# Kernel tuning notes

Hardware: AMD Instinct MI355X
Metric: run time of the kernel (lower is better)

Reference implementation:

```python
import jax, jax.numpy as jnp
import numpy as np

K_MASK = -2.3819763e+38
B, T, D = 1, 2048, 3584
N, KH, H = 28, 4, 128  # query heads, kv heads, head_dim
ROPE_THETA = 1000000.0


def _rope_tables(t, h, theta):
    pos = jnp.arange(t, dtype=jnp.float32)[:, None]
    freq = theta ** (-jnp.arange(0, h, 2, dtype=jnp.float32) / h)[None, :]
    ang = pos * freq  # (T, H/2)
    return jnp.sin(ang)[None], jnp.cos(ang)[None]  # (1, T, H/2)


def apply_rotary_embedding(x, sin, cos):
    # x: (B,T,heads,H); sin/cos: (B,T,H/2)
    x1, x2 = x[..., : x.shape[-1] // 2], x[..., x.shape[-1] // 2 :]
    s, c = sin[:, :, None, :], cos[:, :, None, :]
    return jnp.concatenate([x1 * c - x2 * s, x2 * c + x1 * s], axis=-1)


def setup_inputs() -> dict:
    key = jax.random.key(0)
    ks = jax.random.split(key, 8)
    x = jax.random.normal(ks[0], (B, T, D), jnp.float32)
    attn_mask = jnp.tril(jnp.ones((T, T), jnp.bool_))[None]  # causal (B,T,S)
    sin, cos = _rope_tables(T, H, ROPE_THETA)
    std = 0.02
    wq = jax.random.normal(ks[1], (D, N, H), jnp.float32) * std
    wk = jax.random.normal(ks[2], (D, KH, H), jnp.float32) * std
    wv = jax.random.normal(ks[3], (D, KH, H), jnp.float32) * std
    wo = jax.random.normal(ks[4], (N, H, D), jnp.float32) * std
    q_bias = jax.random.normal(ks[5], (N * H,), jnp.float32) * std
    k_bias = jax.random.normal(ks[6], (KH * H,), jnp.float32) * std
    v_bias = jax.random.normal(ks[7], (KH * H,), jnp.float32) * std
    return {"x": x, "attn_mask": attn_mask, "sin": sin, "cos": cos,
            "wq": wq, "wk": wk, "wv": wv, "wo": wo,
            "q_bias": q_bias, "k_bias": k_bias, "v_bias": v_bias}


def reference(x, attn_mask, sin, cos, wq, wk, wv, wo, q_bias, k_bias, v_bias):
    b, t, _ = x.shape
    q = jnp.einsum('BTD,DNH->BTNH', x, wq) + q_bias.reshape(1, 1, N, H)
    k = jnp.einsum('BSD,DKH->BSKH', x, wk) + k_bias.reshape(1, 1, KH, H)
    v = jnp.einsum('BSD,DKH->BSKH', x, wv) + v_bias.reshape(1, 1, KH, H)
    q = apply_rotary_embedding(q, sin, cos)
    k = apply_rotary_embedding(k, sin, cos)
    g = N // KH  # GQA group size
    scale = H ** -0.5
    qg = q.reshape(b, t, KH, g, H)
    attn = jnp.einsum('BTHGD,BSHD->BHGTS', qg, k) * scale  # no KV repetition
    attn = attn.reshape(b, N, t, t)
    attn = jnp.where(attn_mask[:, None, :, :], attn, K_MASK)
    attn = jax.nn.softmax(attn.astype(jnp.float32), axis=-1).astype(k.dtype)
    attn = attn.reshape(b, KH, g, t, t)
    qkv = jnp.einsum('BHGTS,BSHD->BTHGD', attn, v).reshape(b, t, N, H)
    return jnp.einsum('BTNH,NHD->BTD', qkv, wo)
```

## Files before the change

### kernel.cpp

```cpp
#include <hip/hip_runtime.h>
#include <hip/hip_bf16.h>
#include <math.h>

#define Tn 2048
#define Dn 3584
#define NH 28
#define KHn 4
#define Hn 128
#define Gn 7
#define SCALE 0.08838834764831845f
#define LDC 4608
#define KOFF 3584
#define VOFF 4096
#define FBQ 128
#define FBS 64

typedef unsigned short u16;
typedef __attribute__((ext_vector_type(8))) short short8;
typedef __attribute__((ext_vector_type(4))) float floatx4;

__device__ __forceinline__ float bf_lo(unsigned int u) {
    union { unsigned int i; float f; } x; x.i = u << 16; return x.f;
}
__device__ __forceinline__ u16 f2bf(float f) {
    __hip_bfloat16 h = __float2bfloat16(f);
    return *reinterpret_cast<u16*>(&h);
}

__global__ void cast_f32_bf16(const float* __restrict__ in, u16* __restrict__ out, int n4)
{
    const int idx = blockIdx.x * blockDim.x + threadIdx.x;
    if (idx >= n4) return;
    const float4 f = ((const float4*)in)[idx];
    ((ushort4*)out)[idx] = make_ushort4(f2bf(f.x), f2bf(f.y), f2bf(f.z), f2bf(f.w));
}

__global__ __launch_bounds__(256) void transpose_cast(
    const float* __restrict__ in, u16* __restrict__ out, int R, int C, int ldo)
{
    __shared__ float ts[32][33];
    const int tid = threadIdx.x;
    const int c0 = blockIdx.x * 32, r0 = blockIdx.y * 32;
    const int tx = tid & 31, ty = tid >> 5;
    #pragma unroll
    for (int i = 0; i < 4; ++i)
        ts[ty + i * 8][tx] = in[(size_t)(r0 + ty + i * 8) * C + c0 + tx];
    __syncthreads();
    #pragma unroll
    for (int i = 0; i < 4; ++i)
        out[(size_t)(c0 + ty + i * 8) * ldo + r0 + tx] = f2bf(ts[tx][ty + i * 8]);
}

__global__ __launch_bounds__(256) void transpose_v(
    const u16* __restrict__ qkv, u16* __restrict__ vt)
{
    __shared__ u16 ts[32][33];
    const int tid = threadIdx.x;
    const int s0 = blockIdx.x * 32, d0 = blockIdx.y * 32;
    const int tx = tid & 31, ty = tid >> 5;
    #pragma unroll
    for (int i = 0; i < 4; ++i)
        ts[ty + i * 8][tx] = qkv[(size_t)(s0 + ty + i * 8) * LDC + VOFF + d0 + tx];
    __syncthreads();
    #pragma unroll
    for (int i = 0; i < 4; ++i)
        vt[(size_t)(d0 + ty + i * 8) * Tn + s0 + tx] = ts[tx][ty + i * 8];
}

__global__ void concat_bias(const float* __restrict__ qb, const float* __restrict__ kb,
                            const float* __restrict__ vb, float* __restrict__ out)
{
    const int j = blockIdx.x * blockDim.x + threadIdx.x;
    if (j >= 4608) return;
    out[j] = j < 3584 ? qb[j] : (j < 4096 ? kb[j - 3584] : vb[j - 4096]);
}

#define GM 128
#define GN 128
#define GK 32

__device__ __forceinline__ void async16(const void* g, void* l) {
    __builtin_amdgcn_global_load_lds(
        (const __attribute__((address_space(1))) unsigned int*)g,
        (__attribute__((address_space(3))) unsigned int*)l, 16, 0, 0);
}

template <typename OUT_T>
__global__ __launch_bounds__(256) void gemm_bf16_mfma(
    const u16* __restrict__ A, const u16* __restrict__ Bt,
    const float* __restrict__ bias, OUT_T* __restrict__ C,
    int M, int N, int K, int ldc)
{
    __shared__ __align__(16) u16 As[GM * GK];
    __shared__ __align__(16) u16 Bs[GN * GK];

    const int tid  = threadIdx.x;
    const int lane = tid & 63;
    const int wave = tid >> 6;
    const int wr = wave >> 1, wc = wave & 1;
    const int m16 = lane & 15, quad = lane >> 4;

    const int bm = blockIdx.y * GM;
    const int bn = blockIdx.x * GN;

    floatx4 acc[4][4];
    #pragma unroll
    for (int i = 0; i < 4; ++i)
        #pragma unroll
        for (int j = 0; j < 4; ++j) acc[i][j] = (floatx4)0.f;

    const int rl   = lane >> 2;
    const int kcol = (lane & 3) * 8;

    for (int k0 = 0; k0 < K; k0 += GK) {
        __syncthreads();
        #pragma unroll
        for (int i = 0; i < 2; ++i) {
            const int c = wave + i * 4;
            const int row = c * 16 + rl;
            async16(A  + (size_t)(bm + row) * K + k0 + kcol, &As[c * 512]);
            async16(Bt + (size_t)(bn + row) * K + k0 + kcol, &Bs[c * 512]);
        }
        __builtin_amdgcn_s_waitcnt(0);
        __syncthreads();

        short8 af[4], bfr[4];
        #pragma unroll
        for (int i = 0; i < 4; ++i)
            af[i] = *(const short8*)&As[(wr * 64 + i * 16 + m16) * GK + quad * 8];
        #pragma unroll
        for (int j = 0; j < 4; ++j)
            bfr[j] = *(const short8*)&Bs[(wc * 64 + j * 16 + m16) * GK + quad * 8];
        #pragma unroll
        for (int i = 0; i < 4; ++i)
            #pragma unroll
            for (int j = 0; j < 4; ++j)
                acc[i][j] = __builtin_amdgcn_mfma_f32_16x16x32_bf16(
                    af[i], bfr[j], acc[i][j], 0, 0, 0);
    }

    #pragma unroll
    for (int j = 0; j < 4; ++j) {
        const int col = bn + wc * 64 + j * 16 + m16;
        const float bv = bias ? bias[col] : 0.f;
        #pragma unroll
        for (int i = 0; i < 4; ++i) {
            const int rbase = bm + wr * 64 + i * 16 + quad * 4;
            #pragma unroll
            for (int r = 0; r < 4; ++r) {
                const float v = acc[i][j][r] + bv;
                if constexpr (sizeof(OUT_T) == 2)
                    C[(size_t)(rbase + r) * ldc + col] = (OUT_T)f2bf(v);
                else
                    C[(size_t)(rbase + r) * ldc + col] = v;
            }
        }
    }
}

__global__ void rope_bf16(u16* __restrict__ base,
                          const float* __restrict__ sin_t,
                          const float* __restrict__ cos_t,
                          int heads)
{
    const int idx = blockIdx.x * blockDim.x + threadIdx.x;
    const int n_elem = Tn * heads * 64;
    if (idx >= n_elem) return;
    const int i = idx & 63;
    const int h = (idx >> 6) % heads;
    const int t = idx / (64 * heads);
    const float s = sin_t[t * 64 + i];
    const float c = cos_t[t * 64 + i];
    u16* p = base + (size_t)t * LDC + h * Hn;
    const float x1 = bf_lo((unsigned int)p[i]);
    const float x2 = bf_lo((unsigned int)p[i + 64]);
    p[i]      = f2bf(x1 * c - x2 * s);
    p[i + 64] = f2bf(x2 * c + x1 * s);
}

__global__ __launch_bounds__(256, 2) void flash_attn_mfma(
    const u16* __restrict__ qkv, const u16* __restrict__ vt, u16* __restrict__ o)
{
    const int qt = (int)(gridDim.x - 1 - blockIdx.x);
    const int n  = blockIdx.y;
    const int kh = n / Gn;
    const int tid  = threadIdx.x;
    const int lane = tid & 63;
    const int w    = tid >> 6;
    const int m16  = lane & 15;
    const int quad = lane >> 4;

    __shared__ __align__(16) u16 smem[64 * 136 + 128 * 72 + 128 * 72];
    u16* Ks = smem;
    u16* Vs = smem + 64 * 136;
    u16* Ps = Vs + 128 * 72;
    u16* Os = smem;

    short8 qf[2][4];
    #pragma unroll
    for (int p = 0; p < 2; ++p) {
        const int qrow = qt * FBQ + w * 32 + p * 16 + m16;
        const u16* qp = qkv + (size_t)qrow * LDC + n * Hn;
        #pragma unroll
        for (int kc = 0; kc < 4; ++kc)
            qf[p][kc] = *(const short8*)(qp + kc * 32 + quad * 8);
    }

    floatx4 oacc[2][8];
    #pragma unroll
    for (int p = 0; p < 2; ++p)
        #pragma unroll
        for (int jn = 0; jn < 8; ++jn) oacc[p][jn] = (floatx4)0.f;
    float mrow[2][4], lrow[2][4];
    #pragma unroll
    for (int p = 0; p < 2; ++p)
        #pragma unroll
        for (int r = 0; r < 4; ++r) { mrow[p][r] = -3.0e38f; lrow[p][r] = 0.f; }

    const int krow = tid >> 2, kseg = tid & 3;
    const int vrow = tid >> 1, vseg = tid & 1;
    const int nst = 2 * qt + 2;

    uint4 kv[4], vv[4];
    {
        const u16* kp = qkv + (size_t)(krow) * LDC + KOFF + kh * Hn + kseg * 32;
        #pragma unroll
        for (int i = 0; i < 4; ++i) kv[i] = *(const uint4*)(kp + i * 8);
        const u16* vp = vt + (size_t)(kh * Hn + vrow) * Tn + vseg * 32;
        #pragma unroll
        for (int i = 0; i < 4; ++i) vv[i] = *(const uint4*)(vp + i * 8);
    }

    for (int st = 0; st < nst; ++st) {
        __syncthreads();
        #pragma unroll
        for (int i = 0; i < 4; ++i)
            *(uint4*)&Ks[krow * 136 + kseg * 32 + i * 8] = kv[i];
        #pragma unroll
        for (int i = 0; i < 4; ++i)
            *(uint4*)&Vs[vrow * 72 + vseg * 32 + i * 8] = vv[i];
        __syncthreads();

        {
            const int pst = (st + 1 < nst) ? st + 1 : nst - 1;
            const u16* kp = qkv + (size_t)(pst * FBS + krow) * LDC + KOFF + kh * Hn + kseg * 32;
            #pragma unroll
            for (int i = 0; i < 4; ++i) kv[i] = *(const uint4*)(kp + i * 8);
            const u16* vp = vt + (size_t)(kh * Hn + vrow) * Tn + pst * FBS + vseg * 32;
            #pragma unroll
            for (int i = 0; i < 4; ++i) vv[i] = *(const uint4*)(vp + i * 8);
        }

        const bool active = (st * FBS) <= (qt * FBQ + w * 32 + 31);
        if (active) {
            floatx4 sacc[2][4];
            #pragma unroll
            for (int p = 0; p < 2; ++p)
                #pragma unroll
                for (int j = 0; j < 4; ++j) sacc[p][j] = (floatx4)0.f;
            #pragma unroll
            for (int j = 0; j < 4; ++j) {
                #pragma unroll
                for (int kc = 0; kc < 4; ++kc) {
                    const short8 bfv = *(const short8*)&Ks[(j * 16 + m16) * 136 + kc * 32 + quad * 8];
                    sacc[0][j] = __builtin_amdgcn_mfma_f32_16x16x32_bf16(qf[0][kc], bfv, sacc[0][j], 0, 0, 0);
                    sacc[1][j] = __builtin_amdgcn_mfma_f32_16x16x32_bf16(qf[1][kc], bfv, sacc[1][j], 0, 0, 0);
                }
            }

            const bool diag = (st >= 2 * qt);
            #pragma unroll
            for (int p = 0; p < 2; ++p) {
                #pragma unroll
                for (int r = 0; r < 4; ++r) {
                    const int prow = w * 32 + p * 16 + quad * 4 + r;
                    const int row  = qt * FBQ + prow;
                    float sv[4];
                    #pragma unroll
                    for (int j = 0; j < 4; ++j) {
                        float s = sacc[p][j][r] * SCALE;
                        if (diag && (st * FBS + j * 16 + m16 > row)) s = -1.0e30f;
                        sv[j] = s;
                    }
                    float mx = fmaxf(fmaxf(sv[0], sv[1]), fmaxf(sv[2], sv[3]));
                    mx = fmaxf(mx, __shfl_xor(mx, 1));
                    mx = fmaxf(mx, __shfl_xor(mx, 2));
                    mx = fmaxf(mx, __shfl_xor(mx, 4));
                    mx = fmaxf(mx, __shfl_xor(mx, 8));
                    const float mnew  = fmaxf(mrow[p][r], mx);
                    const float alpha = __expf(mrow[p][r] - mnew);
                    mrow[p][r] = mnew;
                    float ls = 0.f;
                    #pragma unroll
                    for (int j = 0; j < 4; ++j) {
                        const float e = __expf(sv[j] - mnew);
                        ls += e;
                        Ps[prow * 72 + j * 16 + m16] = f2bf(e);
                    }
                    lrow[p][r] = lrow[p][r] * alpha + ls;
                    #pragma unroll
                    for (int jn = 0; jn < 8; ++jn) oacc[p][jn][r] *= alpha;
                }
            }

            #pragma unroll
            for (int kc2 = 0; kc2 < 2; ++kc2) {
                const short8 af0 = *(const short8*)&Ps[(w * 32 + m16) * 72 + kc2 * 32 + quad * 8];
                const short8 af1 = *(const short8*)&Ps[(w * 32 + 16 + m16) * 72 + kc2 * 32 + quad * 8];
                #pragma unroll
                for (int jn = 0; jn < 8; ++jn) {
                    const short8 bfv = *(const short8*)&Vs[(jn * 16 + m16) * 72 + kc2 * 32 + quad * 8];
                    oacc[0][jn] = __builtin_amdgcn_mfma_f32_16x16x32_bf16(af0, bfv, oacc[0][jn], 0, 0, 0);
                    oacc[1][jn] = __builtin_amdgcn_mfma_f32_16x16x32_bf16(af1, bfv, oacc[1][jn], 0, 0, 0);
                }
            }
        }
    }

    float inv[2][4];
    #pragma unroll
    for (int p = 0; p < 2; ++p)
        #pragma unroll
        for (int r = 0; r < 4; ++r) {
            float l = lrow[p][r];
            l += __shfl_xor(l, 1); l += __shfl_xor(l, 2);
            l += __shfl_xor(l, 4); l += __shfl_xor(l, 8);
            inv[p][r] = 1.0f / l;
        }

    __syncthreads();
    #pragma unroll
    for (int p = 0; p < 2; ++p)
        #pragma unroll
        for (int r = 0; r < 4; ++r) {
            const int mrw = w * 32 + p * 16 + quad * 4 + r;
            #pragma unroll
            for (int jn = 0; jn < 8; ++jn)
                Os[mrw * 136 + jn * 16 + m16] = f2bf(oacc[p][jn][r] * inv[p][r]);
        }
    {
        const int mrw  = w * 32 + (lane >> 1);
        const int half = lane & 1;
        const int grow = qt * FBQ + mrw;
        u16* orow = o + (size_t)grow * Dn + n * Hn + half * 64;
        #pragma unroll
        for (int i = 0; i < 8; ++i) {
            const uint4 d = *(const uint4*)&Os[mrw * 136 + half * 64 + i * 8];
            *(uint4*)(orow + i * 8) = d;
        }
    }
}

extern "C" void kernel_launch(void* const* d_in, const int* in_sizes, int n_in,
                              void* d_out, int out_size, void* d_ws, size_t ws_size,
                              hipStream_t stream)
{
    const float* x      = (const float*)d_in[0];
    const float* sin_t  = (const float*)d_in[2];
    const float* cos_t  = (const float*)d_in[3];
    const float* wq     = (const float*)d_in[4];
    const float* wk     = (const float*)d_in[5];
    const float* wv     = (const float*)d_in[6];
    const float* wo     = (const float*)d_in[7];
    const float* q_bias = (const float*)d_in[8];
    const float* k_bias = (const float*)d_in[9];
    const float* v_bias = (const float*)d_in[10];
    float* out = (float*)d_out;

    char* ws = (char*)d_ws;
    u16*  cqkv = (u16*)ws;
    u16*  abuf = (u16*)(ws + 18874368);
    u16*  wt   = (u16*)(ws + 18874368 + 14680064);
    float* bqkv = (float*)(ws + 66584576);
    u16*  vtg  = wt;
    u16*  xb   = (u16*)d_out;

    cast_f32_bf16<<<(Tn * Dn / 4 + 255) / 256, 256, 0, stream>>>(x, xb, Tn * Dn / 4);
    transpose_cast<<<dim3(Dn / 32, Dn / 32), 256, 0, stream>>>(wq, wt, Dn, Dn, Dn);
    transpose_cast<<<dim3(512 / 32, Dn / 32), 256, 0, stream>>>(wk, wt + (size_t)KOFF * Dn, Dn, 512, Dn);
    transpose_cast<<<dim3(512 / 32, Dn / 32), 256, 0, stream>>>(wv, wt + (size_t)VOFF * Dn, Dn, 512, Dn);
    concat_bias<<<18, 256, 0, stream>>>(q_bias, k_bias, v_bias, bqkv);

    gemm_bf16_mfma<u16><<<dim3(LDC / GN, Tn / GM), 256, 0, stream>>>(
        xb, wt, bqkv, cqkv, Tn, LDC, Dn, LDC);

    rope_bf16<<<(Tn * 32 * 64 + 255) / 256, 256, 0, stream>>>(cqkv, sin_t, cos_t, 32);

    transpose_v<<<dim3(Tn / 32, 512 / 32), 256, 0, stream>>>(cqkv, vtg);

    flash_attn_mfma<<<dim3(Tn / FBQ, NH), 256, 0, stream>>>(cqkv, vtg, abuf);

    transpose_cast<<<dim3(Dn / 32, Dn / 32), 256, 0, stream>>>(wo, wt, Dn, Dn, Dn);
    gemm_bf16_mfma<float><<<dim3(Dn / GN, Tn / GM), 256, 0, stream>>>(
        abuf, wt, nullptr, out, Tn, Dn, Dn, Dn);
}
```

Measured before the change: 600.3 us.

## Split flash attention over two key-range halves and merge with combine kernel

The flash attention kernel now splits each query tile's causal key range into two halves across a third grid dimension. Each half writes unnormalized fp32 partial outputs plus per-row max and sum, and a new combine kernel merges them into the bf16 attention buffer. This doubles the number of blocks to improve occupancy and balance the triangular causal workload. The cost is extra fp32 partial-output traffic, roughly 58 MB written and read back, plus an extra launch.

```diff
diff --git a/kernel.cpp b/kernel.cpp
--- a/kernel.cpp
+++ b/kernel.cpp
@@ -14,6 +14,7 @@
 #define VOFF 4096
 #define FBQ 128
 #define FBS 64
+#define NSPLIT 2
 
 typedef unsigned short u16;
 typedef __attribute__((ext_vector_type(8))) short short8;
@@ -179,10 +180,13 @@
 }
 
 __global__ __launch_bounds__(256, 2) void flash_attn_mfma(
-    const u16* __restrict__ qkv, const u16* __restrict__ vt, u16* __restrict__ o)
+    const u16* __restrict__ qkv, const u16* __restrict__ vt,
+    float* __restrict__ po0, float* __restrict__ po1,
+    float2* __restrict__ ml)
 {
     const int qt = (int)(gridDim.x - 1 - blockIdx.x);
     const int n  = blockIdx.y;
+    const int z  = blockIdx.z;
     const int kh = n / Gn;
     const int tid  = threadIdx.x;
     const int lane = tid & 63;
@@ -194,7 +198,6 @@
     u16* Ks = smem;
     u16* Vs = smem + 64 * 136;
     u16* Ps = Vs + 128 * 72;
-    u16* Os = smem;
 
     short8 qf[2][4];
     #pragma unroll
@@ -219,19 +222,20 @@
 
     const int krow = tid >> 2, kseg = tid & 3;
     const int vrow = tid >> 1, vseg = tid & 1;
-    const int nst = 2 * qt + 2;
+    const int st0 = z * (qt + 1);
+    const int st1 = st0 + qt + 1;
 
     uint4 kv[4], vv[4];
     {
-        const u16* kp = qkv + (size_t)(krow) * LDC + KOFF + kh * Hn + kseg * 32;
+        const u16* kp = qkv + (size_t)(st0 * FBS + krow) * LDC + KOFF + kh * Hn + kseg * 32;
         #pragma unroll
         for (int i = 0; i < 4; ++i) kv[i] = *(const uint4*)(kp + i * 8);
-        const u16* vp = vt + (size_t)(kh * Hn + vrow) * Tn + vseg * 32;
+        const u16* vp = vt + (size_t)(kh * Hn + vrow) * Tn + st0 * FBS + vseg * 32;
         #pragma unroll
         for (int i = 0; i < 4; ++i) vv[i] = *(const uint4*)(vp + i * 8);
     }
 
-    for (int st = 0; st < nst; ++st) {
+    for (int st = st0; st < st1; ++st) {
         __syncthreads();
         #pragma unroll
         for (int i = 0; i < 4; ++i)
@@ -242,7 +246,7 @@
         __syncthreads();
 
         {
-            const int pst = (st + 1 < nst) ? st + 1 : nst - 1;
+            const int pst = (st + 1 < st1) ? st + 1 : st1 - 1;
             const u16* kp = qkv + (size_t)(pst * FBS + krow) * LDC + KOFF + kh * Hn + kseg * 32;
             #pragma unroll
             for (int i = 0; i < 4; ++i) kv[i] = *(const uint4*)(kp + i * 8);
@@ -317,7 +321,7 @@
         }
     }
 
-    float inv[2][4];
+    float lsum[2][4];
     #pragma unroll
     for (int p = 0; p < 2; ++p)
         #pragma unroll
@@ -325,30 +329,58 @@
             float l = lrow[p][r];
             l += __shfl_xor(l, 1); l += __shfl_xor(l, 2);
             l += __shfl_xor(l, 4); l += __shfl_xor(l, 8);
-            inv[p][r] = 1.0f / l;
-        }
-
-    __syncthreads();
+            lsum[p][r] = l;
+        }
+
+    if (m16 == 0) {
+        #pragma unroll
+        for (int p = 0; p < 2; ++p)
+            #pragma unroll
+            for (int r = 0; r < 4; ++r) {
+                const int row = qt * FBQ + w * 32 + p * 16 + quad * 4 + r;
+                ml[((size_t)z * NH + n) * Tn + row] = make_float2(mrow[p][r], lsum[p][r]);
+            }
+    }
+
+    float* po = z ? po1 : po0;
     #pragma unroll
     for (int p = 0; p < 2; ++p)
         #pragma unroll
         for (int r = 0; r < 4; ++r) {
-            const int mrw = w * 32 + p * 16 + quad * 4 + r;
+            const int grow = qt * FBQ + w * 32 + p * 16 + quad * 4 + r;
+            float* pr = po + (size_t)grow * Dn + n * Hn + m16;
             #pragma unroll
             for (int jn = 0; jn < 8; ++jn)
-                Os[mrw * 136 + jn * 16 + m16] = f2bf(oacc[p][jn][r] * inv[p][r]);
-        }
-    {
-        const int mrw  = w * 32 + (lane >> 1);
-        const int half = lane & 1;
-        const int grow = qt * FBQ + mrw;
-        u16* orow = o + (size_t)grow * Dn + n * Hn + half * 64;
-        #pragma unroll
-        for (int i = 0; i < 8; ++i) {
-            const uint4 d = *(const uint4*)&Os[mrw * 136 + half * 64 + i * 8];
-            *(uint4*)(orow + i * 8) = d;
-        }
-    }
+                pr[jn * 16] = oacc[p][jn][r];
+        }
+}
+
+__global__ __launch_bounds__(256) void combine_splits(
+    const float* __restrict__ po0, const float* __restrict__ po1,
+    const float2* __restrict__ ml, u16* __restrict__ ob)
+{
+    const int idx = blockIdx.x * blockDim.x + threadIdx.x;
+    const int n4  = Tn * Dn / 4;
+    if (idx >= n4) return;
+    const int c4  = idx % (Dn / 4);
+    const int row = idx / (Dn / 4);
+    const int n   = (c4 * 4) / Hn;
+
+    const float2 ml0 = ml[(size_t)n * Tn + row];
+    const float2 ml1 = ml[(size_t)(NH + n) * Tn + row];
+    const float  M   = fmaxf(ml0.x, ml1.x);
+    const float  a0  = __expf(ml0.x - M);
+    const float  a1  = __expf(ml1.x - M);
+    const float  dn_ = 1.0f / (ml0.y * a0 + ml1.y * a1);
+
+    const float4 v0 = ((const float4*)po0)[idx];
+    const float4 v1 = ((const float4*)po1)[idx];
+    ushort4 o;
+    o.x = f2bf((v0.x * a0 + v1.x * a1) * dn_);
+    o.y = f2bf((v0.y * a0 + v1.y * a1) * dn_);
+    o.z = f2bf((v0.z * a0 + v1.z * a1) * dn_);
+    o.w = f2bf((v0.w * a0 + v1.w * a1) * dn_);
+    ((ushort4*)ob)[idx] = o;
 }
 
 extern "C" void kernel_launch(void* const* d_in, const int* in_sizes, int n_in,
@@ -373,6 +405,9 @@
     u16*  wt   = (u16*)(ws + 18874368 + 14680064);
     float* bqkv = (float*)(ws + 66584576);
     u16*  vtg  = wt;
+    float* po0 = (float*)d_out;
+    float* po1 = (float*)(ws + 35651584);
+    float2* mlb = (float2*)(ws + 65011712);
     u16*  xb   = (u16*)d_out;
 
     cast_f32_bf16<<<(Tn * Dn / 4 + 255) / 256, 256, 0, stream>>>(x, xb, Tn * Dn / 4);
@@ -388,7 +423,10 @@
 
     transpose_v<<<dim3(Tn / 32, 512 / 32), 256, 0, stream>>>(cqkv, vtg);
 
-    flash_attn_mfma<<<dim3(Tn / FBQ, NH), 256, 0, stream>>>(cqkv, vtg, abuf);
+    flash_attn_mfma<<<dim3(Tn / FBQ, NH, NSPLIT), 256, 0, stream>>>(
+        cqkv, vtg, po0, po1, mlb);
+
+    combine_splits<<<(Tn * Dn / 4 + 255) / 256, 256, 0, stream>>>(po0, po1, mlb, abuf);
 
     transpose_cast<<<dim3(Dn / 32, Dn / 32), 256, 0, stream>>>(wo, wt, Dn, Dn, Dn);
     gemm_bf16_mfma<float><<<dim3(Dn / GN, Tn / GM), 256, 0, stream>>>(
```

After: 621.0 us. 3.4% more time.
